# Kernel tuning notes

Hardware: AMD Instinct MI355X
Metric: run time of the kernel (lower is better)

## Reference

```python
import jax, jax.numpy as jnp
import numpy as np

GRID_SIZE = 5
ORDER = 3  # spline_order
H_STEP = 2.0 / GRID_SIZE  # grid_range = [-1, 1]
GRID = jnp.arange(-ORDER, GRID_SIZE + ORDER + 1, dtype=jnp.float32) * H_STEP - 1.0  # (12,)


def b_splines(x):
    # x: (N, F) -> bases: (N, F, GRID_SIZE + ORDER) via Cox-de Boor recursion
    g = GRID
    xx = x[..., None]
    bases = ((xx >= g[:-1]) & (xx < g[1:])).astype(x.dtype)
    for k in range(1, ORDER + 1):
        left = (xx - g[:-(k + 1)]) / (g[k:-1] - g[:-(k + 1)]) * bases[..., :-1]
        right = (g[k + 1:] - xx) / (g[k + 1:] - g[1:-k]) * bases[..., 1:]
        bases = left + right
    return bases


def kan_linear(x, bw, sw, sc):
    # x: (N, F); bw: (O, F); sw: (O, F, C); sc: (O, F)
    base = jax.nn.silu(x) @ bw.T
    spline = jnp.einsum('nfc,ofc->no', b_splines(x), sw * sc[..., None])
    return base + spline


def kan_conv(x, bw, sw, sc):
    # x: (B, C, H, W); 3x3 patches, padding 1, stride 1 -> KANLinear over C*9 features
    B, C, H, W = x.shape
    patches = jax.lax.conv_general_dilated_patches(x, (3, 3), (1, 1), ((1, 1), (1, 1)))  # (B, C*9, H, W)
    p = patches.transpose(0, 2, 3, 1).reshape(B * H * W, C * 9)
    o = kan_linear(p, bw, sw, sc)  # (B*H*W, Cout)
    return o.reshape(B, H, W, -1).transpose(0, 3, 1, 2)


def maxpool2(x):
    B, C, H, W = x.shape
    return x.reshape(B, C, H // 2, 2, W // 2, 2).max(axis=(3, 5))


def setup_inputs() -> dict:
    key = jax.random.key(0)
    ks = jax.random.split(key, 32)
    d = {}
    d['x'] = jax.random.normal(ks[0], (128, 3, 32, 32), dtype=jnp.float32)
    conv_specs = [(3, 4), (4, 8), (8, 16), (16, 32)]
    i = 1
    for li, (cin, cout) in enumerate(conv_specs, 1):
        fin = cin * 9
        d[f'bw{li}'] = jax.random.normal(ks[i], (cout, fin), dtype=jnp.float32) * (1.0 / np.sqrt(fin)); i += 1
        d[f'sw{li}'] = jax.random.normal(ks[i], (cout, fin, GRID_SIZE + ORDER), dtype=jnp.float32) * 0.1; i += 1
        d[f'sc{li}'] = jax.random.normal(ks[i], (cout, fin), dtype=jnp.float32) * (1.0 / np.sqrt(fin)); i += 1
    lin_specs = [(2048, 2048), (1024, 2048), (10, 1024)]
    for li, (o, inn) in enumerate(lin_specs, 1):
        d[f'w{li}'] = jax.random.normal(ks[i], (o, inn), dtype=jnp.float32) * (1.0 / np.sqrt(inn)); i += 1
        d[f'b{li}'] = jnp.zeros((o,), dtype=jnp.float32); i += 1
    return d


def reference(x, bw1, sw1, sc1, bw2, sw2, sc2, bw3, sw3, sc3, bw4, sw4, sc4, w1, b1, w2, b2, w3, b3):
    x = kan_conv(x, bw1, sw1, sc1)
    x = kan_conv(x, bw2, sw2, sc2)
    x = maxpool2(x)
    x = kan_conv(x, bw3, sw3, sc3)
    x = kan_conv(x, bw4, sw4, sc4)
    x = maxpool2(x)
    x = x.reshape(x.shape[0], -1)  # (B, 32*8*8)
    x = jax.nn.relu(x @ w1.T + b1)
    x = jax.nn.relu(x @ w2.T + b2)
    return x @ w3.T + b3
```

## Files before the change

kernel.cpp:

```cpp
#include <hip/hip_runtime.h>
#include <hip/hip_bf16.h>

#define BATCH 128
#define AST 88

typedef __attribute__((ext_vector_type(8))) short bf16x8;
typedef __attribute__((ext_vector_type(16))) float f32x16;

__device__ __forceinline__ void spline_acts(float xv, float act[9]) {
    act[0] = xv * (1.0f / (1.0f + __expf(-xv)));
    float g[12];
#pragma unroll
    for (int i = 0; i < 12; ++i) g[i] = (float)(i - 3) * 0.4f - 1.0f;
    float bb[11];
#pragma unroll
    for (int c = 0; c < 11; ++c) bb[c] = (xv >= g[c] && xv < g[c + 1]) ? 1.0f : 0.0f;
#pragma unroll
    for (int k = 1; k <= 3; ++k) {
#pragma unroll
        for (int c = 0; c + k < 11; ++c) {
            float left  = (xv - g[c]) * (1.0f / (g[c + k] - g[c])) * bb[c];
            float right = (g[c + k + 1] - xv) * (1.0f / (g[c + k + 1] - g[c + 1])) * bb[c + 1];
            bb[c] = left + right;
        }
    }
#pragma unroll
    for (int c = 0; c < 8; ++c) act[c + 1] = bb[c];
}

__device__ __constant__ float ZPAD[9] = {0.0f, 0.0f, 0.0f, 0.02083333333f,
                                         0.47916666667f, 0.47916666667f,
                                         0.02083333333f, 0.0f, 0.0f};

__device__ __forceinline__ void bf16split(float x, ushort& h, ushort& l) {
    __hip_bfloat16 bh = __float2bfloat16(x);
    float hf = __bfloat162float(bh);
    __hip_bfloat16 bl = __float2bfloat16(x - hf);
    h = *(ushort*)&bh;
    l = *(ushort*)&bl;
}

__device__ __forceinline__ float wval(const float* bw, const float* sw, const float* sc,
                                      int F, int f, int j, int o) {
    if (j == 0) return bw[o * F + f];
    return sw[(o * F + f) * 8 + (j - 1)] * sc[o * F + f];
}

__global__ __launch_bounds__(256) void prep_kernel(
    const float* __restrict__ bw1, const float* __restrict__ sw1, const float* __restrict__ sc1,
    const float* __restrict__ bw2, const float* __restrict__ sw2, const float* __restrict__ sc2,
    const float* __restrict__ bw3, const float* __restrict__ sw3, const float* __restrict__ sc3,
    const float* __restrict__ bw4, const float* __restrict__ sw4, const float* __restrict__ sc4,
    ushort* __restrict__ k1h, ushort* __restrict__ k1l,
    ushort* __restrict__ k2h, ushort* __restrict__ k2l,
    ushort* __restrict__ k3h, ushort* __restrict__ k3l,
    ushort* __restrict__ k4h, ushort* __restrict__ k4l,
    ushort* __restrict__ zph, ushort* __restrict__ zpl) {
    int i = blockIdx.x * 256 + threadIdx.x;
    if (i < 1152) {
        int l = i & 63, s = (i >> 6) & 1, t = i / 128;
#pragma unroll
        for (int e = 0; e < 8; ++e) {
            int k = s * 16 + ((l >> 5) * 8) + e, o = l & 31;
            float w = 0.f;
            if (k < 27 && o < 4) w = wval(bw1, sw1, sc1, 27, (k / 9) * 9 + t, k % 9, o);
            ushort h, lo; bf16split(w, h, lo);
            k1h[i * 8 + e] = h; k1l[i * 8 + e] = lo;
        }
    } else if (i < 2880) {
        int q = i - 1152;
        int l = q & 63, s = (q >> 6) % 3, t = q / 192;
#pragma unroll
        for (int e = 0; e < 8; ++e) {
            int k = s * 16 + ((l >> 5) * 8) + e, o = l & 31;
            float w = 0.f;
            if (k < 36 && o < 8) w = wval(bw2, sw2, sc2, 36, (k / 9) * 9 + t, k % 9, o);
            ushort h, lo; bf16split(w, h, lo);
            k2h[q * 8 + e] = h; k2l[q * 8 + e] = lo;
        }
    } else if (i < 5760) {
        int q = i - 2880;
        int l = q & 63, s = (q >> 6) % 5, t = q / 320;
#pragma unroll
        for (int e = 0; e < 8; ++e) {
            int k = s * 16 + ((l >> 5) * 8) + e, o = l & 31;
            float w = 0.f;
            if (k < 72 && o < 16) w = wval(bw3, sw3, sc3, 72, (k / 9) * 9 + t, k % 9, o);
            ushort h, lo; bf16split(w, h, lo);
            k3h[q * 8 + e] = h; k3l[q * 8 + e] = lo;
        }
    } else if (i < 11520) {
        int q = i - 5760;
        int l = q & 63, s = (q >> 6) % 5, t = (q / 320) % 9, p = q / 2880;
#pragma unroll
        for (int e = 0; e < 8; ++e) {
            int k = s * 16 + ((l >> 5) * 8) + e, o = l & 31;
            float w = 0.f;
            if (k < 72) w = wval(bw4, sw4, sc4, 144, (p * 8 + k / 9) * 9 + t, k % 9, o);
            ushort h, lo; bf16split(w, h, lo);
            k4h[q * 8 + e] = h; k4l[q * 8 + e] = lo;
        }
    } else if (i < 11600) {
        int c = i - 11520;
        ushort h, lo; bf16split(ZPAD[c % 9], h, lo);
        zph[c] = h; zpl[c] = lo;
    }
}

__global__ __launch_bounds__(256) void conv1_fused(
    const float* __restrict__ x,
    const ushort* __restrict__ Bgh, const ushort* __restrict__ Bgl,
    ushort* __restrict__ Oh, ushort* __restrict__ Ol) {
    constexpr int ASTR = 40, KSTEPS = 2, NCO = 4;
    __shared__ ushort AH[204 * ASTR];
    __shared__ ushort AL[204 * ASTR];
    const int tid = threadIdx.x;
    const int b = blockIdx.x >> 3, strip = blockIdx.x & 7;
    const int r0 = strip * 4;
    const int lane = tid & 63, wv = tid >> 6;

    for (int px = tid; px < 204; px += 256) {
        int lr = px / 34, pc = px - lr * 34;
        int grow = r0 - 1 + lr, gc = pc - 1;
        bool inb = ((unsigned)grow < 32u) && ((unsigned)gc < 32u);
        unsigned rh[16], rl[16];
#pragma unroll
        for (int w = 0; w < 16; ++w) { rh[w] = 0u; rl[w] = 0u; }
        if (inb) {
            const float* xb = x + (size_t)b * 3072 + grow * 32 + gc;
#pragma unroll
            for (int cin = 0; cin < 3; ++cin) {
                float a9[9];
                spline_acts(xb[cin * 1024], a9);
#pragma unroll
                for (int j = 0; j < 9; ++j) {
                    ushort h, l2; bf16split(a9[j], h, l2);
                    int c = cin * 9 + j;
                    if (c & 1) { rh[c >> 1] |= (unsigned)h << 16; rl[c >> 1] |= (unsigned)l2 << 16; }
                    else       { rh[c >> 1] |= h;                  rl[c >> 1] |= l2; }
                }
            }
        } else {
#pragma unroll
            for (int c = 0; c < 27; ++c) {
                ushort h, l2; bf16split(ZPAD[c % 9], h, l2);
                if (c & 1) { rh[c >> 1] |= (unsigned)h << 16; rl[c >> 1] |= (unsigned)l2 << 16; }
                else       { rh[c >> 1] |= h;                  rl[c >> 1] |= l2; }
            }
        }
        unsigned* dh = (unsigned*)&AH[px * ASTR];
        unsigned* dl = (unsigned*)&AL[px * ASTR];
#pragma unroll
        for (int w = 0; w < 16; ++w) { dh[w] = rh[w]; dl[w] = rl[w]; }
    }
    __syncthreads();

    f32x16 acc;
#pragma unroll
    for (int i = 0; i < 16; ++i) acc[i] = 0.f;

    const int p0 = wv * 32 + (lane & 31);
    const int sp0 = ((p0 >> 5) + 1) * 34 + (p0 & 31) + 1;
    const int koff = (lane >> 5) * 8;

#pragma unroll 1
    for (int t = 0; t < 9; ++t) {
        const int dA = ((t / 3) - 1) * 34 + (t % 3) - 1;
#pragma unroll
        for (int s = 0; s < KSTEPS; ++s) {
            bf16x8 ah = *(const bf16x8*)(&AH[(sp0 + dA) * ASTR + s * 16 + koff]);
            bf16x8 al = *(const bf16x8*)(&AL[(sp0 + dA) * ASTR + s * 16 + koff]);
            bf16x8 bh = *(const bf16x8*)(Bgh + (size_t)((t * KSTEPS + s) * 64 + lane) * 8);
            bf16x8 bl = *(const bf16x8*)(Bgl + (size_t)((t * KSTEPS + s) * 64 + lane) * 8);
            acc = __builtin_amdgcn_mfma_f32_32x32x16_bf16(ah, bh, acc, 0, 0, 0);
            acc = __builtin_amdgcn_mfma_f32_32x32x16_bf16(ah, bl, acc, 0, 0, 0);
            acc = __builtin_amdgcn_mfma_f32_32x32x16_bf16(al, bh, acc, 0, 0, 0);
        }
    }
    __syncthreads();

    float* fl = (float*)AH;
    {
        int ccol = lane & 31;
        if (ccol < NCO) {
#pragma unroll
            for (int r = 0; r < 16; ++r) {
                int row = (r & 3) + 8 * (r >> 2) + 4 * (lane >> 5);
                fl[ccol * 129 + wv * 32 + row] = acc[r];
            }
        }
    }
    __syncthreads();

    unsigned* ubh = (unsigned*)AL;
    unsigned* ubl = (unsigned*)AH + 1032;
    {
        int px = tid >> 1, cop = tid & 1;
        unsigned rwh[9], rwl[9];
#pragma unroll
        for (int w = 0; w < 9; ++w) { rwh[w] = 0u; rwl[w] = 0u; }
#pragma unroll
        for (int e = 0; e < 2; ++e) {
            int co = cop * 2 + e;
            float a9[9];
            spline_acts(fl[co * 129 + px], a9);
#pragma unroll
            for (int j = 0; j < 9; ++j) {
                ushort h, l2; bf16split(a9[j], h, l2);
                int c = e * 9 + j;
                if (c & 1) { rwh[c >> 1] |= (unsigned)h << 16; rwl[c >> 1] |= (unsigned)l2 << 16; }
                else       { rwh[c >> 1] |= h;                  rwl[c >> 1] |= l2; }
            }
        }
#pragma unroll
        for (int w = 0; w < 9; ++w) {
            ubh[px * 18 + cop * 9 + w] = rwh[w];
            ubl[px * 18 + cop * 9 + w] = rwl[w];
        }
    }
    __syncthreads();
    size_t basew = ((size_t)b * 1024 + strip * 128) * 18;
    unsigned* goh = (unsigned*)Oh + basew;
    unsigned* gol = (unsigned*)Ol + basew;
#pragma unroll
    for (int e = 0; e < 9; ++e) {
        int q = e * 256 + tid;
        goh[q] = ubh[q];
        gol[q] = ubl[q];
    }
}

template <int KG, int CHG, int CHL, int ASTR, int KSTEPS, int NCO>
__global__ __launch_bounds__(256) void conv2_strip(
    const ushort* __restrict__ Agh, const ushort* __restrict__ Agl,
    const ushort* __restrict__ Bgh, const ushort* __restrict__ Bgl,
    const ushort* __restrict__ zph, const ushort* __restrict__ zpl,
    ushort* __restrict__ Oh, ushort* __restrict__ Ol) {
    __shared__ ushort AH[340 * ASTR];
    __shared__ ushort AL[340 * ASTR];
    const int tid = threadIdx.x;
    const int b = blockIdx.x >> 2, strip = blockIdx.x & 3;
    const int r0 = strip * 8;
    const int lane = tid & 63, wv = tid >> 6;

    {
        const ushort* ash = Agh + (size_t)b * 1024 * KG;
        const ushort* asl = Agl + (size_t)b * 1024 * KG;
        for (int idx = tid; idx < 320 * CHL; idx += 256) {
            int pxl = idx / CHL, ch = idx - pxl * CHL;
            int lr = pxl >> 5, c = pxl & 31;
            int grow = r0 - 1 + lr;
            uint2 vh, vl;
            if (ch >= CHG) { vh = make_uint2(0u, 0u); vl = make_uint2(0u, 0u); }
            else if ((unsigned)grow < 32u) {
                vh = *(const uint2*)(ash + (size_t)(grow * 32 + c) * KG + ch * 4);
                vl = *(const uint2*)(asl + (size_t)(grow * 32 + c) * KG + ch * 4);
            } else {
                vh = *(const uint2*)(zph + ch * 4);
                vl = *(const uint2*)(zpl + ch * 4);
            }
            int spx = lr * 34 + c + 1;
            *(uint2*)(&AH[spx * ASTR + ch * 4]) = vh;
            *(uint2*)(&AL[spx * ASTR + ch * 4]) = vl;
        }
        for (int idx = tid; idx < 20 * CHL; idx += 256) {
            int sel = idx / CHL, ch = idx - sel * CHL;
            int lr = sel >> 1, c = (sel & 1) ? 33 : 0;
            int spx = lr * 34 + c;
            uint2 vh, vl;
            if (ch >= CHG) { vh = make_uint2(0u, 0u); vl = make_uint2(0u, 0u); }
            else { vh = *(const uint2*)(zph + ch * 4); vl = *(const uint2*)(zpl + ch * 4); }
            *(uint2*)(&AH[spx * ASTR + ch * 4]) = vh;
            *(uint2*)(&AL[spx * ASTR + ch * 4]) = vl;
        }
    }
    __syncthreads();

    f32x16 acc0, acc1;
#pragma unroll
    for (int i = 0; i < 16; ++i) { acc0[i] = 0.f; acc1[i] = 0.f; }

    const int p0 = wv * 64 + (lane & 31);
    const int sp0 = ((p0 >> 5) + 1) * 34 + (p0 & 31) + 1;
    const int sp1 = sp0 + 34;
    const int koff = (lane >> 5) * 8;

#pragma unroll 1
    for (int t = 0; t < 9; ++t) {
        const int dA = ((t / 3) - 1) * 34 + (t % 3) - 1;
#pragma unroll
        for (int s = 0; s < KSTEPS; ++s) {
            bf16x8 a0h = *(const bf16x8*)(&AH[(sp0 + dA) * ASTR + s * 16 + koff]);
            bf16x8 a0l = *(const bf16x8*)(&AL[(sp0 + dA) * ASTR + s * 16 + koff]);
            bf16x8 a1h = *(const bf16x8*)(&AH[(sp1 + dA) * ASTR + s * 16 + koff]);
            bf16x8 a1l = *(const bf16x8*)(&AL[(sp1 + dA) * ASTR + s * 16 + koff]);
            bf16x8 bh = *(const bf16x8*)(Bgh + (size_t)((t * KSTEPS + s) * 64 + lane) * 8);
            bf16x8 bl = *(const bf16x8*)(Bgl + (size_t)((t * KSTEPS + s) * 64 + lane) * 8);
            acc0 = __builtin_amdgcn_mfma_f32_32x32x16_bf16(a0h, bh, acc0, 0, 0, 0);
            acc1 = __builtin_amdgcn_mfma_f32_32x32x16_bf16(a1h, bh, acc1, 0, 0, 0);
            acc0 = __builtin_amdgcn_mfma_f32_32x32x16_bf16(a0h, bl, acc0, 0, 0, 0);
            acc1 = __builtin_amdgcn_mfma_f32_32x32x16_bf16(a1h, bl, acc1, 0, 0, 0);
            acc0 = __builtin_amdgcn_mfma_f32_32x32x16_bf16(a0l, bh, acc0, 0, 0, 0);
            acc1 = __builtin_amdgcn_mfma_f32_32x32x16_bf16(a1l, bh, acc1, 0, 0, 0);
        }
    }
    __syncthreads();

    float* fl = (float*)AH;
    {
        int ccol = lane & 31;
        if (ccol < NCO) {
#pragma unroll
            for (int r = 0; r < 16; ++r) {
                int row = (r & 3) + 8 * (r >> 2) + 4 * (lane >> 5);
                fl[ccol * 257 + wv * 64 + row] = acc0[r];
                fl[ccol * 257 + wv * 64 + 32 + row] = acc1[r];
            }
        }
    }
    __syncthreads();

    int cg = tid >> 6, pl = tid & 63;
    int phl = pl >> 4, pw = pl & 15;
    int base_m = (2 * phl) * 32 + 2 * pw;
    unsigned rwh[9], rwl[9];
#pragma unroll
    for (int w = 0; w < 9; ++w) { rwh[w] = 0u; rwl[w] = 0u; }
#pragma unroll
    for (int e = 0; e < 2; ++e) {
        int co = cg * 2 + e;
        const float* fb = fl + co * 257 + base_m;
        float m = fmaxf(fmaxf(fb[0], fb[1]), fmaxf(fb[32], fb[33]));
        float a9[9];
        spline_acts(m, a9);
#pragma unroll
        for (int j = 0; j < 9; ++j) {
            ushort h, l2; bf16split(a9[j], h, l2);
            int c = e * 9 + j;
            if (c & 1) { rwh[c >> 1] |= (unsigned)h << 16; rwl[c >> 1] |= (unsigned)l2 << 16; }
            else       { rwh[c >> 1] |= h;                  rwl[c >> 1] |= l2; }
        }
    }
    unsigned* ubh = (unsigned*)AL;
    unsigned* ubl = (unsigned*)AL + 2560;
#pragma unroll
    for (int w = 0; w < 9; ++w) {
        ubh[pl * 40 + cg * 9 + w] = rwh[w];
        ubl[pl * 40 + cg * 9 + w] = rwl[w];
    }
    if (cg == 3) {
#pragma unroll
        for (int w = 0; w < 4; ++w) { ubh[pl * 40 + 36 + w] = 0u; ubl[pl * 40 + 36 + w] = 0u; }
    }
    __syncthreads();
    size_t base = ((size_t)b * 256 + strip * 64) * 80;
    const ushort* sbh = (const ushort*)ubh;
    const ushort* sbl = (const ushort*)ubl;
#pragma unroll
    for (int e = 0; e < 3; ++e) {
        int q = e * 256 + tid;
        if (q < 640) {
            *(uint4*)(Oh + base + q * 8) = *(const uint4*)(sbh + q * 8);
            *(uint4*)(Ol + base + q * 8) = *(const uint4*)(sbl + q * 8);
        }
    }
}

template <int NPH, int NCO>
__global__ __launch_bounds__(256) void conv34_part(
    const ushort* __restrict__ Agh, const ushort* __restrict__ Agl,
    const ushort* __restrict__ Bgh, const ushort* __restrict__ Bgl,
    const ushort* __restrict__ zph, const ushort* __restrict__ zpl,
    float* __restrict__ P) {
    __shared__ ushort AH[144 * AST];
    __shared__ ushort AL[144 * AST];
    const int tid = threadIdx.x;
    const int b = blockIdx.x, half = blockIdx.y, g = blockIdx.z;
    const int r0 = half * 8;
    const int lane = tid & 63, wv = tid >> 6;

    f32x16 acc;
#pragma unroll
    for (int i = 0; i < 16; ++i) acc[i] = 0.f;

    const int m = wv * 32 + (lane & 31);
    const int sbase = (m >> 4) * 18 + (m & 15);
    const int koff = (lane >> 5) * 8;

#pragma unroll 1
    for (int p = 0; p < NPH; ++p) {
        if (p) __syncthreads();
        const ushort* ash = Agh + ((size_t)b * NPH + p) * 256 * 80;
        const ushort* asl = Agl + ((size_t)b * NPH + p) * 256 * 80;
#pragma unroll
        for (int e = 0; e < 6; ++e) {
            int idx = e * 256 + tid;
            if (idx < 1440) {
                int px = idx / 10, ch = idx - px * 10;
                int pr = px / 18, pc = px - pr * 18;
                int r = r0 - 1 + g + pr, c = pc - 1;
                bool inb = ((unsigned)r < 16u) && ((unsigned)c < 16u);
                uint4 vh, vl;
                if (inb) {
                    vh = *(const uint4*)(ash + (size_t)(r * 16 + c) * 80 + ch * 8);
                    vl = *(const uint4*)(asl + (size_t)(r * 16 + c) * 80 + ch * 8);
                } else {
                    vh = *(const uint4*)(zph + ch * 8);
                    vl = *(const uint4*)(zpl + ch * 8);
                }
                *(uint4*)(&AH[px * AST + ch * 8]) = vh;
                *(uint4*)(&AL[px * AST + ch * 8]) = vl;
            }
        }
        __syncthreads();

        const ushort* bsh = Bgh + (size_t)p * 2880 * 8;
        const ushort* bsl = Bgl + (size_t)p * 2880 * 8;
#pragma unroll
        for (int dw = 0; dw < 3; ++dw) {
            const int t = g * 3 + dw;
#pragma unroll
            for (int s = 0; s < 5; ++s) {
                bf16x8 ah = *(const bf16x8*)(&AH[(sbase + dw) * AST + s * 16 + koff]);
                bf16x8 al = *(const bf16x8*)(&AL[(sbase + dw) * AST + s * 16 + koff]);
                bf16x8 bh = *(const bf16x8*)(bsh + (size_t)((t * 5 + s) * 64 + lane) * 8);
                bf16x8 bl = *(const bf16x8*)(bsl + (size_t)((t * 5 + s) * 64 + lane) * 8);
                acc = __builtin_amdgcn_mfma_f32_32x32x16_bf16(ah, bh, acc, 0, 0, 0);
                acc = __builtin_amdgcn_mfma_f32_32x32x16_bf16(ah, bl, acc, 0, 0, 0);
                acc = __builtin_amdgcn_mfma_f32_32x32x16_bf16(al, bh, acc, 0, 0, 0);
            }
        }
    }

    int co = lane & 31;
    if (co < NCO) {
        float* pb = P + ((size_t)(g * 256 + b * 2 + half) * 128) * NCO;
#pragma unroll
        for (int r = 0; r < 16; ++r) {
            int px = wv * 32 + (r & 3) + 8 * (r >> 2) + 4 * (lane >> 5);
            pb[px * NCO + co] = acc[r];
        }
    }
}

__global__ __launch_bounds__(256) void conv3_reduce(const float* __restrict__ P3,
                                                    ushort* __restrict__ A4h,
                                                    ushort* __restrict__ A4l) {
    __shared__ ushort SBH[2][64 * 80];
    __shared__ ushort SBL[2][64 * 80];
    int b = blockIdx.x, pxq = blockIdx.y;
    int t = threadIdx.x;
    int co = t & 15, pxg = t >> 4;
#pragma unroll
    for (int q = 0; q < 4; ++q) {
        int lpx64 = pxg * 4 + q;
        int px = pxq * 64 + lpx64;
        int bh = b * 2 + (px >> 7), lpx = px & 127;
        float s = 0.f;
#pragma unroll
        for (int zz = 0; zz < 3; ++zz)
            s += P3[((size_t)(zz * 256 + bh) * 128 + lpx) * 16 + co];
        float a9[9];
        spline_acts(s, a9);
        int ph = co >> 3, c8 = co & 7;
#pragma unroll
        for (int j = 0; j < 9; ++j) {
            ushort h, l2; bf16split(a9[j], h, l2);
            SBH[ph][lpx64 * 80 + c8 * 9 + j] = h;
            SBL[ph][lpx64 * 80 + c8 * 9 + j] = l2;
        }
        if (c8 == 7) {
#pragma unroll
            for (int w = 0; w < 8; ++w) {
                SBH[ph][lpx64 * 80 + 72 + w] = 0;
                SBL[ph][lpx64 * 80 + 72 + w] = 0;
            }
        }
    }
    __syncthreads();
#pragma unroll
    for (int ph = 0; ph < 2; ++ph) {
        size_t base = ((size_t)(b * 2 + ph) * 256 + pxq * 64) * 80;
#pragma unroll
        for (int e = 0; e < 3; ++e) {
            int q = e * 256 + t;
            if (q < 640) {
                *(uint4*)(A4h + base + q * 8) = *(const uint4*)(&SBH[ph][q * 8]);
                *(uint4*)(A4l + base + q * 8) = *(const uint4*)(&SBL[ph][q * 8]);
            }
        }
    }
}

__global__ __launch_bounds__(256) void conv4_reduce_pool(const float* __restrict__ P4,
                                                         float* __restrict__ pooled) {
    __shared__ float SM[32 * 33];
    int b = blockIdx.x, half = blockIdx.y;
    int t = threadIdx.x;
    int co = t & 31, pg = t >> 5;
    int bh = b * 2 + half;
#pragma unroll
    for (int q = 0; q < 4; ++q) {
        int pp = pg * 4 + q;
        int lr = pp >> 3, pc = pp & 7;
        int px00 = (2 * lr) * 16 + 2 * pc;
        float s00 = 0.f, s01 = 0.f, s10 = 0.f, s11 = 0.f;
#pragma unroll
        for (int zz = 0; zz < 3; ++zz) {
            const float* pb = P4 + ((size_t)(zz * 256 + bh) * 128) * 32 + co;
            s00 += pb[(size_t)px00 * 32];
            s01 += pb[(size_t)(px00 + 1) * 32];
            s10 += pb[(size_t)(px00 + 16) * 32];
            s11 += pb[(size_t)(px00 + 17) * 32];
        }
        SM[co * 33 + pp] = fmaxf(fmaxf(s00, s01), fmaxf(s10, s11));
    }
    __syncthreads();
#pragma unroll
    for (int e = 0; e < 4; ++e) {
        int idx = e * 256 + t;
        int co2 = idx >> 5, pp2 = idx & 31;
        int lr2 = pp2 >> 3, pc2 = pp2 & 7;
        pooled[(size_t)b * 2048 + co2 * 64 + (half * 4 + lr2) * 8 + pc2] = SM[co2 * 33 + pp2];
    }
}

template <int SPLIT>
__global__ __launch_bounds__(256) void fc_big(const float* __restrict__ A,
                                              const float* __restrict__ Wt,
                                              float* __restrict__ part,
                                              int M, int N, int K) {
    __shared__ float As[32][68];
    __shared__ float Ws[32][68];
    const int tid = threadIdx.x;
    const int tx = tid & 15, ty = tid >> 4;
    const int bm = blockIdx.y * 64, bn = blockIdx.x * 64;
    const int kc = K / SPLIT;
    const int kbeg = blockIdx.z * kc;
    float acc[4][4] = {};
    for (int k0 = kbeg; k0 < kbeg + kc; k0 += 32) {
#pragma unroll
        for (int e = 0; e < 2; ++e) {
            int q = e * 256 + tid;
            int r = q >> 3, k4 = (q & 7) * 4;
            float4 av = *(const float4*)&A[(size_t)(bm + r) * K + k0 + k4];
            float4 wv = *(const float4*)&Wt[(size_t)(bn + r) * K + k0 + k4];
            As[k4 + 0][r] = av.x; As[k4 + 1][r] = av.y;
            As[k4 + 2][r] = av.z; As[k4 + 3][r] = av.w;
            Ws[k4 + 0][r] = wv.x; Ws[k4 + 1][r] = wv.y;
            Ws[k4 + 2][r] = wv.z; Ws[k4 + 3][r] = wv.w;
        }
        __syncthreads();
#pragma unroll
        for (int kk = 0; kk < 32; ++kk) {
            float4 av = *(const float4*)(&As[kk][ty * 4]);
            float4 wv = *(const float4*)(&Ws[kk][tx * 4]);
            acc[0][0] = fmaf(av.x, wv.x, acc[0][0]);
            acc[0][1] = fmaf(av.x, wv.y, acc[0][1]);
            acc[0][2] = fmaf(av.x, wv.z, acc[0][2]);
            acc[0][3] = fmaf(av.x, wv.w, acc[0][3]);
            acc[1][0] = fmaf(av.y, wv.x, acc[1][0]);
            acc[1][1] = fmaf(av.y, wv.y, acc[1][1]);
            acc[1][2] = fmaf(av.y, wv.z, acc[1][2]);
            acc[1][3] = fmaf(av.y, wv.w, acc[1][3]);
            acc[2][0] = fmaf(av.z, wv.x, acc[2][0]);
            acc[2][1] = fmaf(av.z, wv.y, acc[2][1]);
            acc[2][2] = fmaf(av.z, wv.z, acc[2][2]);
            acc[2][3] = fmaf(av.z, wv.w, acc[2][3]);
            acc[3][0] = fmaf(av.w, wv.x, acc[3][0]);
            acc[3][1] = fmaf(av.w, wv.y, acc[3][1]);
            acc[3][2] = fmaf(av.w, wv.z, acc[3][2]);
            acc[3][3] = fmaf(av.w, wv.w, acc[3][3]);
        }
        __syncthreads();
    }
    float* p = part + (size_t)blockIdx.z * M * N;
#pragma unroll
    for (int i = 0; i < 4; ++i) {
        float4 v = make_float4(acc[i][0], acc[i][1], acc[i][2], acc[i][3]);
        *(float4*)&p[(size_t)(bm + ty * 4 + i) * N + (bn + tx * 4)] = v;
    }
}

template <int SPLIT>
__global__ void fc_reduce(const float* __restrict__ part, const float* __restrict__ bias,
                          float* __restrict__ C, int MN, int N, int relu) {
    int i = blockIdx.x * 256 + threadIdx.x;
    if (i >= MN) return;
    float s = bias[i % N];
#pragma unroll
    for (int z = 0; z < SPLIT; ++z) s += part[(size_t)z * MN + i];
    C[i] = relu ? fmaxf(s, 0.f) : s;
}

__global__ __launch_bounds__(256) void fc3_kernel(const float* __restrict__ A,
                                                  const float* __restrict__ Wt,
                                                  const float* __restrict__ bias,
                                                  float* __restrict__ C) {
    int gid = blockIdx.x * 256 + threadIdx.x;
    int wid = gid >> 6;
    int lane = gid & 63;
    int m = wid / 10, n = wid - m * 10;
    const float4* a = (const float4*)(A + (size_t)m * 1024);
    const float4* w = (const float4*)(Wt + (size_t)n * 1024);
    float s = 0.f;
#pragma unroll
    for (int it = 0; it < 4; ++it) {
        float4 av = a[it * 64 + lane];
        float4 wv = w[it * 64 + lane];
        s += av.x * wv.x + av.y * wv.y + av.z * wv.z + av.w * wv.w;
    }
#pragma unroll
    for (int off = 32; off; off >>= 1) s += __shfl_xor(s, off);
    if (lane == 0) C[wid] = s + bias[n];
}

extern "C" void kernel_launch(void* const* d_in, const int* in_sizes, int n_in,
                              void* d_out, int out_size, void* d_ws, size_t ws_size,
                              hipStream_t stream) {
    const float* x   = (const float*)d_in[0];
    const float* bw1 = (const float*)d_in[1];
    const float* sw1 = (const float*)d_in[2];
    const float* sc1 = (const float*)d_in[3];
    const float* bw2 = (const float*)d_in[4];
    const float* sw2 = (const float*)d_in[5];
    const float* sc2 = (const float*)d_in[6];
    const float* bw3 = (const float*)d_in[7];
    const float* sw3 = (const float*)d_in[8];
    const float* sc3 = (const float*)d_in[9];
    const float* bw4 = (const float*)d_in[10];
    const float* sw4 = (const float*)d_in[11];
    const float* sc4 = (const float*)d_in[12];
    const float* w1  = (const float*)d_in[13];
    const float* b1  = (const float*)d_in[14];
    const float* w2  = (const float*)d_in[15];
    const float* b2  = (const float*)d_in[16];
    const float* w3  = (const float*)d_in[17];
    const float* b3  = (const float*)d_in[18];

    float*  wsf = (float*)d_ws;
    ushort* wsu = (ushort*)d_ws;
    ushort* k1h = wsu + 110848;
    ushort* k1l = wsu + 120064;
    ushort* k2h = wsu + 129280;
    ushort* k2l = wsu + 143104;
    ushort* k3h = wsu + 156928;
    ushort* k3l = wsu + 179968;
    ushort* k4h = wsu + 203008;
    ushort* k4l = wsu + 249088;
    ushort* zph = wsu + 295168;
    ushort* zpl = wsu + 295248;
    ushort* A2h = wsu + 7864320;
    ushort* A2l = wsu + 12582912;
    ushort* A3h = wsu + 524288;
    ushort* A3l = wsu + 3145728;
    ushort* A4h = wsu + 5767168;
    ushort* A4l = wsu + 11010048;
    float* P3   = wsf + 9437184;
    float* P4   = wsf + 11534336;
    float* pooled = wsf + 262144;
    float* part1  = wsf + 524288;
    float* fc1o   = wsf + 2621440;
    float* part2  = wsf + 2883584;
    float* fc2o   = wsf + 3932160;

    prep_kernel<<<46, 256, 0, stream>>>(bw1, sw1, sc1, bw2, sw2, sc2,
                                        bw3, sw3, sc3, bw4, sw4, sc4,
                                        k1h, k1l, k2h, k2l, k3h, k3l, k4h, k4l,
                                        zph, zpl);

    conv1_fused<<<1024, 256, 0, stream>>>(x, k1h, k1l, A2h, A2l);
    conv2_strip<36, 9, 12, 56, 3, 8><<<512, 256, 0, stream>>>(A2h, A2l, k2h, k2l,
                                                              zph, zpl, A3h, A3l);
    conv34_part<1, 16><<<dim3(128, 2, 3), 256, 0, stream>>>(A3h, A3l, k3h, k3l,
                                                            zph, zpl, P3);
    conv3_reduce<<<dim3(128, 4), 256, 0, stream>>>(P3, A4h, A4l);
    conv34_part<2, 32><<<dim3(128, 2, 3), 256, 0, stream>>>(A4h, A4l, k4h, k4l,
                                                            zph, zpl, P4);
    conv4_reduce_pool<<<dim3(128, 2), 256, 0, stream>>>(P4, pooled);

    fc_big<8><<<dim3(32, 2, 8), 256, 0, stream>>>(pooled, w1, part1, 128, 2048, 2048);
    fc_reduce<8><<<1024, 256, 0, stream>>>(part1, b1, fc1o, 262144, 2048, 1);
    fc_big<8><<<dim3(16, 2, 8), 256, 0, stream>>>(fc1o, w2, part2, 128, 1024, 2048);
    fc_reduce<8><<<512, 256, 0, stream>>>(part2, b2, fc2o, 131072, 1024, 1);
    fc3_kernel<<<320, 256, 0, stream>>>(fc2o, w3, b3, (float*)d_out);
}
```

Baseline: 129.2 us.

## Split conv2 into 4-row strips with one MFMA accumulator per wave

The conv2 kernel now processes 4 output rows per block instead of 8, launching 1024 blocks instead of 512. Each wave computes one 32-pixel tile instead of two. The halo load is unified into a single loop over a 34-wide padded tile, and the pool/spline epilogue maps one thread per (channel, pooled pixel). The aim is more blocks and less shared memory per block for better occupancy and load balance, at the cost of extra halo reloading (6 rows loaded for 4 output rows) and less B-fragment reuse per load.

```diff
diff --git a/kernel.cpp b/kernel.cpp
--- a/kernel.cpp
+++ b/kernel.cpp
@@ -230,59 +230,48 @@
     }
 }
 
-template <int KG, int CHG, int CHL, int ASTR, int KSTEPS, int NCO>
-__global__ __launch_bounds__(256) void conv2_strip(
+__global__ __launch_bounds__(256) void conv2_strip4(
     const ushort* __restrict__ Agh, const ushort* __restrict__ Agl,
     const ushort* __restrict__ Bgh, const ushort* __restrict__ Bgl,
     const ushort* __restrict__ zph, const ushort* __restrict__ zpl,
     ushort* __restrict__ Oh, ushort* __restrict__ Ol) {
-    __shared__ ushort AH[340 * ASTR];
-    __shared__ ushort AL[340 * ASTR];
+    constexpr int ASTR = 56, KSTEPS = 3, NCO = 8, CHG = 9, CHL = 12;
+    __shared__ ushort AH[204 * ASTR];
+    __shared__ ushort AL[204 * ASTR];
     const int tid = threadIdx.x;
-    const int b = blockIdx.x >> 2, strip = blockIdx.x & 3;
-    const int r0 = strip * 8;
+    const int b = blockIdx.x >> 3, strip = blockIdx.x & 7;
+    const int r0 = strip * 4;
     const int lane = tid & 63, wv = tid >> 6;
 
     {
-        const ushort* ash = Agh + (size_t)b * 1024 * KG;
-        const ushort* asl = Agl + (size_t)b * 1024 * KG;
-        for (int idx = tid; idx < 320 * CHL; idx += 256) {
+        const ushort* ash = Agh + (size_t)b * 1024 * 36;
+        const ushort* asl = Agl + (size_t)b * 1024 * 36;
+        for (int idx = tid; idx < 204 * CHL; idx += 256) {
             int pxl = idx / CHL, ch = idx - pxl * CHL;
-            int lr = pxl >> 5, c = pxl & 31;
-            int grow = r0 - 1 + lr;
+            int lr = pxl / 34, pc = pxl - lr * 34;
+            int grow = r0 - 1 + lr, gc = pc - 1;
+            bool inb = ((unsigned)grow < 32u) && ((unsigned)gc < 32u);
             uint2 vh, vl;
             if (ch >= CHG) { vh = make_uint2(0u, 0u); vl = make_uint2(0u, 0u); }
-            else if ((unsigned)grow < 32u) {
-                vh = *(const uint2*)(ash + (size_t)(grow * 32 + c) * KG + ch * 4);
-                vl = *(const uint2*)(asl + (size_t)(grow * 32 + c) * KG + ch * 4);
+            else if (inb) {
+                vh = *(const uint2*)(ash + (size_t)(grow * 32 + gc) * 36 + ch * 4);
+                vl = *(const uint2*)(asl + (size_t)(grow * 32 + gc) * 36 + ch * 4);
             } else {
                 vh = *(const uint2*)(zph + ch * 4);
                 vl = *(const uint2*)(zpl + ch * 4);
             }
-            int spx = lr * 34 + c + 1;
-            *(uint2*)(&AH[spx * ASTR + ch * 4]) = vh;
-            *(uint2*)(&AL[spx * ASTR + ch * 4]) = vl;
-        }
-        for (int idx = tid; idx < 20 * CHL; idx += 256) {
-            int sel = idx / CHL, ch = idx - sel * CHL;
-            int lr = sel >> 1, c = (sel & 1) ? 33 : 0;
-            int spx = lr * 34 + c;
-            uint2 vh, vl;
-            if (ch >= CHG) { vh = make_uint2(0u, 0u); vl = make_uint2(0u, 0u); }
-            else { vh = *(const uint2*)(zph + ch * 4); vl = *(const uint2*)(zpl + ch * 4); }
-            *(uint2*)(&AH[spx * ASTR + ch * 4]) = vh;
-            *(uint2*)(&AL[spx * ASTR + ch * 4]) = vl;
-        }
-    }
-    __syncthreads();
-
-    f32x16 acc0, acc1;
-#pragma unroll
-    for (int i = 0; i < 16; ++i) { acc0[i] = 0.f; acc1[i] = 0.f; }
-
-    const int p0 = wv * 64 + (lane & 31);
+            *(uint2*)(&AH[pxl * ASTR + ch * 4]) = vh;
+            *(uint2*)(&AL[pxl * ASTR + ch * 4]) = vl;
+        }
+    }
+    __syncthreads();
+
+    f32x16 acc;
+#pragma unroll
+    for (int i = 0; i < 16; ++i) acc[i] = 0.f;
+
+    const int p0 = wv * 32 + (lane & 31);
     const int sp0 = ((p0 >> 5) + 1) * 34 + (p0 & 31) + 1;
-    const int sp1 = sp0 + 34;
     const int koff = (lane >> 5) * 8;
 
 #pragma unroll 1
@@ -290,18 +279,13 @@
         const int dA = ((t / 3) - 1) * 34 + (t % 3) - 1;
 #pragma unroll
         for (int s = 0; s < KSTEPS; ++s) {
-            bf16x8 a0h = *(const bf16x8*)(&AH[(sp0 + dA) * ASTR + s * 16 + koff]);
-            bf16x8 a0l = *(const bf16x8*)(&AL[(sp0 + dA) * ASTR + s * 16 + koff]);
-            bf16x8 a1h = *(const bf16x8*)(&AH[(sp1 + dA) * ASTR + s * 16 + koff]);
-            bf16x8 a1l = *(const bf16x8*)(&AL[(sp1 + dA) * ASTR + s * 16 + koff]);
+            bf16x8 ah = *(const bf16x8*)(&AH[(sp0 + dA) * ASTR + s * 16 + koff]);
+            bf16x8 al = *(const bf16x8*)(&AL[(sp0 + dA) * ASTR + s * 16 + koff]);
             bf16x8 bh = *(const bf16x8*)(Bgh + (size_t)((t * KSTEPS + s) * 64 + lane) * 8);
             bf16x8 bl = *(const bf16x8*)(Bgl + (size_t)((t * KSTEPS + s) * 64 + lane) * 8);
-            acc0 = __builtin_amdgcn_mfma_f32_32x32x16_bf16(a0h, bh, acc0, 0, 0, 0);
-            acc1 = __builtin_amdgcn_mfma_f32_32x32x16_bf16(a1h, bh, acc1, 0, 0, 0);
-            acc0 = __builtin_amdgcn_mfma_f32_32x32x16_bf16(a0h, bl, acc0, 0, 0, 0);
-            acc1 = __builtin_amdgcn_mfma_f32_32x32x16_bf16(a1h, bl, acc1, 0, 0, 0);
-            acc0 = __builtin_amdgcn_mfma_f32_32x32x16_bf16(a0l, bh, acc0, 0, 0, 0);
-            acc1 = __builtin_amdgcn_mfma_f32_32x32x16_bf16(a1l, bh, acc1, 0, 0, 0);
+            acc = __builtin_amdgcn_mfma_f32_32x32x16_bf16(ah, bh, acc, 0, 0, 0);
+            acc = __builtin_amdgcn_mfma_f32_32x32x16_bf16(ah, bl, acc, 0, 0, 0);
+            acc = __builtin_amdgcn_mfma_f32_32x32x16_bf16(al, bh, acc, 0, 0, 0);
         }
     }
     __syncthreads();
@@ -313,53 +297,45 @@
 #pragma unroll
             for (int r = 0; r < 16; ++r) {
                 int row = (r & 3) + 8 * (r >> 2) + 4 * (lane >> 5);
-                fl[ccol * 257 + wv * 64 + row] = acc0[r];
-                fl[ccol * 257 + wv * 64 + 32 + row] = acc1[r];
-            }
-        }
-    }
-    __syncthreads();
-
-    int cg = tid >> 6, pl = tid & 63;
-    int phl = pl >> 4, pw = pl & 15;
-    int base_m = (2 * phl) * 32 + 2 * pw;
-    unsigned rwh[9], rwl[9];
-#pragma unroll
-    for (int w = 0; w < 9; ++w) { rwh[w] = 0u; rwl[w] = 0u; }
-#pragma unroll
-    for (int e = 0; e < 2; ++e) {
-        int co = cg * 2 + e;
-        const float* fb = fl + co * 257 + base_m;
+                fl[ccol * 129 + wv * 32 + row] = acc[r];
+            }
+        }
+    }
+    __syncthreads();
+
+    unsigned* ubh = (unsigned*)AL;
+    unsigned* ubl = (unsigned*)AL + 1280;
+    {
+        int co = tid >> 5, pl = tid & 31;
+        int prl = pl >> 4, pw = pl & 15;
+        int base_m = (2 * prl) * 32 + 2 * pw;
+        const float* fb = fl + co * 129 + base_m;
         float m = fmaxf(fmaxf(fb[0], fb[1]), fmaxf(fb[32], fb[33]));
         float a9[9];
         spline_acts(m, a9);
+        ushort* bh2 = (ushort*)ubh + pl * 80 + co * 9;
+        ushort* bl2 = (ushort*)ubl + pl * 80 + co * 9;
 #pragma unroll
         for (int j = 0; j < 9; ++j) {
             ushort h, l2; bf16split(a9[j], h, l2);
-            int c = e * 9 + j;
-            if (c & 1) { rwh[c >> 1] |= (unsigned)h << 16; rwl[c >> 1] |= (unsigned)l2 << 16; }
-            else       { rwh[c >> 1] |= h;                  rwl[c >> 1] |= l2; }
-        }
-    }
-    unsigned* ubh = (unsigned*)AL;
-    unsigned* ubl = (unsigned*)AL + 2560;
-#pragma unroll
-    for (int w = 0; w < 9; ++w) {
-        ubh[pl * 40 + cg * 9 + w] = rwh[w];
-        ubl[pl * 40 + cg * 9 + w] = rwl[w];
-    }
-    if (cg == 3) {
-#pragma unroll
-        for (int w = 0; w < 4; ++w) { ubh[pl * 40 + 36 + w] = 0u; ubl[pl * 40 + 36 + w] = 0u; }
-    }
-    __syncthreads();
-    size_t base = ((size_t)b * 256 + strip * 64) * 80;
+            bh2[j] = h;
+            bl2[j] = l2;
+        }
+        if (co == 7) {
+            ushort* ph2 = (ushort*)ubh + pl * 80 + 72;
+            ushort* pl2 = (ushort*)ubl + pl * 80 + 72;
+#pragma unroll
+            for (int w = 0; w < 8; ++w) { ph2[w] = 0; pl2[w] = 0; }
+        }
+    }
+    __syncthreads();
+    size_t base = ((size_t)b * 256 + strip * 32) * 80;
     const ushort* sbh = (const ushort*)ubh;
     const ushort* sbl = (const ushort*)ubl;
 #pragma unroll
-    for (int e = 0; e < 3; ++e) {
+    for (int e = 0; e < 2; ++e) {
         int q = e * 256 + tid;
-        if (q < 640) {
+        if (q < 320) {
             *(uint4*)(Oh + base + q * 8) = *(const uint4*)(sbh + q * 8);
             *(uint4*)(Ol + base + q * 8) = *(const uint4*)(sbl + q * 8);
         }
@@ -670,8 +646,7 @@
                                         zph, zpl);
 
     conv1_fused<<<1024, 256, 0, stream>>>(x, k1h, k1l, A2h, A2l);
-    conv2_strip<36, 9, 12, 56, 3, 8><<<512, 256, 0, stream>>>(A2h, A2l, k2h, k2l,
-                                                              zph, zpl, A3h, A3l);
+    conv2_strip4<<<1024, 256, 0, stream>>>(A2h, A2l, k2h, k2l, zph, zpl, A3h, A3l);
     conv34_part<1, 16><<<dim3(128, 2, 3), 256, 0, stream>>>(A3h, A3l, k3h, k3l,
                                                             zph, zpl, P3);
     conv3_reduce<<<dim3(128, 4), 256, 0, stream>>>(P3, A4h, A4l);
```

After: 134.2 us. +3.8%, slower.
